# Kernel optimization log

Hardware: AMD Instinct MI355X
Metric: run time of the kernel (lower is better)

Reference implementation:

```python
import jax, jax.numpy as jnp
import numpy as np

C_IN = 128
C_INNER = 128


def setup_inputs() -> dict:
    key = jax.random.key(0)
    ks = jax.random.split(key, 9)
    b, c, h, w = 4, C_IN, 64, 64
    s = 1.0 / np.sqrt(c)
    x = jax.random.normal(ks[0], (b, c, h, w), dtype=jnp.float32)
    Wq = jax.random.normal(ks[1], (C_INNER, C_IN), dtype=jnp.float32) * s
    bq = jnp.zeros((C_INNER,), dtype=jnp.float32)
    Wk = jax.random.normal(ks[2], (C_INNER, C_IN), dtype=jnp.float32) * s
    bk = jnp.zeros((C_INNER,), dtype=jnp.float32)
    Wv = jax.random.normal(ks[3], (C_INNER, C_IN), dtype=jnp.float32) * s
    bv = jnp.zeros((C_INNER,), dtype=jnp.float32)
    Wo = jax.random.normal(ks[4], (C_IN, C_INNER), dtype=jnp.float32) * (1.0 / np.sqrt(C_INNER))
    bo = jnp.zeros((C_IN,), dtype=jnp.float32)
    return {"x": x, "Wq": Wq, "bq": bq, "Wk": Wk, "bk": bk,
            "Wv": Wv, "bv": bv, "Wo": Wo, "bo": bo}


def _conv1x1(x, W, bias):
    # x: (b,c,h,w), W: (o,c) -> (b,o,h,w)
    return jnp.einsum('oc,bchw->bohw', W, x) + bias[None, :, None, None]


def reference(x, Wq, bq, Wk, bk, Wv, bv, Wo, bo):
    b, c, h, w = x.shape
    ci = Wq.shape[0]
    n = h * w
    q = _conv1x1(x, Wq, bq).reshape(b, ci, n)          # (b, ci, n)
    k = _conv1x1(x, Wk, bk).reshape(b, ci, n)          # (b, ci, n)
    v = _conv1x1(x, Wv, bv).reshape(b, ci, n)          # (b, ci, n)
    # attn = softmax(q^T @ k) over keys
    attn = jnp.einsum('bci,bcj->bij', q, k)            # (b, n, n)
    attn = jax.nn.softmax(attn, axis=-1)
    out = jnp.einsum('bij,bcj->bci', attn, v)          # (b, ci, n)
    out = out.reshape(b, ci, h, w)
    out = _conv1x1(out, Wo, bo)
    return out + x
```

## Files before the change

### kernel.cpp

```cpp
#include <hip/hip_runtime.h>
#include <math.h>
#include <stdint.h>

#define CDIM 128
#define NTOT 4096
#define LOG2E 1.44269504f

typedef _Float16 f16x8 __attribute__((ext_vector_type(8)));
typedef float floatx4 __attribute__((ext_vector_type(4)));

static __device__ __forceinline__ floatx4 mfma16(f16x8 a, f16x8 b, floatx4 c) {
    return __builtin_amdgcn_mfma_f32_16x16x32_f16(a, b, c, 0, 0, 0);
}
static __device__ __forceinline__ unsigned short f2h(float f) {
    _Float16 h = (_Float16)f;
    return __builtin_bit_cast(unsigned short, h);
}
static __device__ __forceinline__ float h2f(unsigned short u) {
    return (float)__builtin_bit_cast(_Float16, u);
}
static __device__ __forceinline__ float fexp2(float x) {
#if __has_builtin(__builtin_amdgcn_exp2f)
    return __builtin_amdgcn_exp2f(x);
#else
    return exp2f(x);
#endif
}

#define SWZ(row, cc) ((((row) << 7)) + ((((cc) ^ ((row) & 15))) << 3))
#define SWZ8(row, cc) ((((row) << 6)) + ((((cc) ^ ((row) & 7))) << 3))

static __device__ __forceinline__ void gload_lds16(const void* g, void* l) {
    __builtin_amdgcn_global_load_lds(
        (const __attribute__((address_space(1))) void*)g,
        (__attribute__((address_space(3))) void*)l, 16, 0, 0);
}

__global__ __launch_bounds__(256) void qkv_proj_kernel(
    const float* __restrict__ x,
    const float* __restrict__ Wq, const float* __restrict__ Wk,
    const float* __restrict__ Wv,
    const float* __restrict__ bq, const float* __restrict__ bk,
    const float* __restrict__ bv,
    unsigned short* __restrict__ qo, unsigned short* __restrict__ ko,
    unsigned short* __restrict__ vo)
{
    __shared__ __align__(16) unsigned short Xs[64][136];
    __shared__ __align__(16) unsigned short Ws[3][64][136];

    const int t = threadIdx.x, b = blockIdx.y, n0 = blockIdx.x * 64;
    const int zo = blockIdx.z * 64;
    const int w = t >> 6, quad = (t >> 4) & 3, l15 = t & 15;

    {
        const int n = (t & 15) * 4;
        const int c = (t >> 4) * 8;
        float4 xr[8];
        #pragma unroll
        for (int j = 0; j < 8; ++j)
            xr[j] = *(const float4*)&x[((size_t)b * CDIM + c + j) * NTOT + n0 + n];
        #pragma unroll
        for (int k = 0; k < 4; ++k) {
            ushort4 ulo, uhi;
            ulo.x = f2h(((const float*)&xr[0])[k]);
            ulo.y = f2h(((const float*)&xr[1])[k]);
            ulo.z = f2h(((const float*)&xr[2])[k]);
            ulo.w = f2h(((const float*)&xr[3])[k]);
            uhi.x = f2h(((const float*)&xr[4])[k]);
            uhi.y = f2h(((const float*)&xr[5])[k]);
            uhi.z = f2h(((const float*)&xr[6])[k]);
            uhi.w = f2h(((const float*)&xr[7])[k]);
            *(ushort4*)&Xs[n + k][c]     = ulo;
            *(ushort4*)&Xs[n + k][c + 4] = uhi;
        }
    }
    {
        const int o = t >> 2, ch = (t & 3) * 32;
        #pragma unroll
        for (int s = 0; s < 3; ++s) {
            const float* W = (s == 0) ? Wq : (s == 1) ? Wk : Wv;
            #pragma unroll
            for (int i = 0; i < 8; ++i) {
                float4 f4 = *(const float4*)&W[(size_t)(zo + o) * CDIM + ch + i * 4];
                ushort4 u = { f2h(f4.x), f2h(f4.y), f2h(f4.z), f2h(f4.w) };
                *(ushort4*)&Ws[s][o][ch + i * 4] = u;
            }
        }
    }
    __syncthreads();

    f16x8 xf[4];
    #pragma unroll
    for (int f = 0; f < 4; ++f)
        xf[f] = *(const f16x8*)&Xs[w * 16 + l15][f * 32 + quad * 8];

    #pragma unroll
    for (int s = 0; s < 2; ++s) {
        const float* bias = s ? bk : bq;
        unsigned short* dst = s ? ko : qo;
        const float sc = (s == 0) ? LOG2E : 1.0f;
        #pragma unroll
        for (int ot = 0; ot < 4; ++ot) {
            floatx4 acc = (floatx4){0.f, 0.f, 0.f, 0.f};
            #pragma unroll
            for (int f = 0; f < 4; ++f) {
                f16x8 aW = *(const f16x8*)&Ws[s][ot * 16 + l15][f * 32 + quad * 8];
                acc = mfma16(aW, xf[f], acc);
            }
            const int ob = zo + ot * 16 + quad * 4;
            ushort4 u;
            u.x = f2h((acc[0] + bias[ob + 0]) * sc);
            u.y = f2h((acc[1] + bias[ob + 1]) * sc);
            u.z = f2h((acc[2] + bias[ob + 2]) * sc);
            u.w = f2h((acc[3] + bias[ob + 3]) * sc);
            *(ushort4*)&dst[((size_t)b * NTOT + n0 + w * 16 + l15) * CDIM + ob] = u;
        }
    }
    #pragma unroll
    for (int ot = 0; ot < 4; ++ot) {
        floatx4 acc = (floatx4){0.f, 0.f, 0.f, 0.f};
        #pragma unroll
        for (int f = 0; f < 4; ++f) {
            f16x8 bW = *(const f16x8*)&Ws[2][ot * 16 + l15][f * 32 + quad * 8];
            acc = mfma16(xf[f], bW, acc);
        }
        const int o = zo + ot * 16 + l15;
        const float bv_ = bv[o];
        ushort4 u;
        u.x = f2h(acc[0] + bv_); u.y = f2h(acc[1] + bv_);
        u.z = f2h(acc[2] + bv_); u.w = f2h(acc[3] + bv_);
        *(ushort4*)&vo[((size_t)b * CDIM + o) * NTOT + n0 + w * 16 + quad * 4] = u;
    }
}

__global__ __launch_bounds__(256, 2) void attn_kernel(
    const unsigned short* __restrict__ qg,
    const unsigned short* __restrict__ kg,
    const unsigned short* __restrict__ vg,
    unsigned short* __restrict__ Op,
    float* __restrict__ Ms, float* __restrict__ Ls)
{
    __shared__ __align__(16) unsigned short Kb[2][64 * 128];
    __shared__ __align__(16) unsigned short Vb[2][128 * 64];
    __shared__ __align__(16) unsigned short Ps[128 * 64];

    const int t = threadIdx.x;
    const int w = t >> 6, quad = (t >> 4) & 3, l15 = t & 15;

    const int bid = blockIdx.x;
    const int swz = ((bid & 7) << 6) | (bid >> 3);
    const int gidx = swz >> 5;
    const int b = gidx & 3;
    const int z = gidx >> 2;
    const int i0 = (swz & 31) * 128;
    const int jbase = z * 1024;
    const size_t vbase = (size_t)b * CDIM * NTOT;

    f16x8 bQ[2][4];
    #pragma unroll
    for (int nt = 0; nt < 2; ++nt) {
        const size_t qrow = ((size_t)b * NTOT + i0 + w * 32 + nt * 16 + l15) * CDIM;
        #pragma unroll
        for (int f = 0; f < 4; ++f)
            bQ[nt][f] = *(const f16x8*)&qg[qrow + f * 32 + quad * 8];
    }

    auto stageK = [&](unsigned short* Kd, int j0) {
        const size_t kbase = ((size_t)b * NTOT + j0) * CDIM;
        #pragma unroll
        for (int r = 0; r < 4; ++r) {
            const int flat = r * 256 + t;
            const int ldsoff = (r * 256 + (t & ~63)) * 8;
            const int krow = flat >> 4, kcc = flat & 15;
            gload_lds16(&kg[kbase + (size_t)krow * CDIM + ((kcc ^ (krow & 15)) << 3)],
                        &Kd[ldsoff]);
        }
    };
    auto stageV = [&](unsigned short* Vd, int j0) {
        const size_t vrow0 = vbase + j0;
        #pragma unroll
        for (int r = 0; r < 4; ++r) {
            const int flat = r * 256 + t;
            const int ldsoff = (r * 256 + (t & ~63)) * 8;
            const int vrow = flat >> 3, vcc = flat & 7;
            gload_lds16(&vg[vrow0 + (size_t)vrow * NTOT + ((vcc ^ (vrow & 7)) << 3)],
                        &Vd[ldsoff]);
        }
    };

    floatx4 accO[2][8];
    #pragma unroll
    for (int nt = 0; nt < 2; ++nt)
        #pragma unroll
        for (int dt = 0; dt < 8; ++dt) accO[nt][dt] = (floatx4){0.f, 0.f, 0.f, 0.f};
    float m_run[2] = {-INFINITY, -INFINITY};
    float l_part[2] = {0.f, 0.f};

    floatx4 accT[2][4];
    uint2 pu[2][4];
    f16x8 bP[2][2];

    auto QK = [&](const unsigned short* Kd) {
        #pragma unroll
        for (int nt = 0; nt < 2; ++nt)
            #pragma unroll
            for (int jt = 0; jt < 4; ++jt) accT[nt][jt] = (floatx4){0.f, 0.f, 0.f, 0.f};
        __builtin_amdgcn_s_setprio(1);
        #pragma unroll
        for (int jt = 0; jt < 4; ++jt)
            #pragma unroll
            for (int f = 0; f < 4; ++f) {
                f16x8 aK = *(const f16x8*)&Kd[SWZ(jt * 16 + l15, f * 4 + quad)];
                accT[0][jt] = mfma16(aK, bQ[0][f], accT[0][jt]);
                accT[1][jt] = mfma16(aK, bQ[1][f], accT[1][jt]);
            }
        __builtin_amdgcn_s_setprio(0);
    };
    auto RB = [&]() {
        #pragma unroll
        for (int nt = 0; nt < 2; ++nt) {
            const int prow = w * 32 + nt * 16 + l15;
            #pragma unroll
            for (int kb = 0; kb < 2; ++kb)
                bP[nt][kb] = *(const f16x8*)&Ps[SWZ8(prow, kb * 4 + quad)];
        }
    };
    auto PV = [&](const unsigned short* Vd) {
        __builtin_amdgcn_s_setprio(1);
        #pragma unroll
        for (int dt = 0; dt < 8; ++dt)
            #pragma unroll
            for (int kb = 0; kb < 2; ++kb) {
                f16x8 aV = *(const f16x8*)&Vd[SWZ8(dt * 16 + l15, kb * 4 + quad)];
                accO[0][dt] = mfma16(aV, bP[0][kb], accO[0][dt]);
                accO[1][dt] = mfma16(aV, bP[1][kb], accO[1][dt]);
            }
        __builtin_amdgcn_s_setprio(0);
    };
    auto SM = [&]() {
        #pragma unroll
        for (int nt = 0; nt < 2; ++nt) {
            float tm = accT[nt][0][0];
            #pragma unroll
            for (int jt = 0; jt < 4; ++jt)
                #pragma unroll
                for (int r = 0; r < 4; ++r) tm = fmaxf(tm, accT[nt][jt][r]);
            tm = fmaxf(tm, __shfl_xor(tm, 16));
            tm = fmaxf(tm, __shfl_xor(tm, 32));
            if (__ballot(tm > m_run[nt] + 11.5416f)) {
                const float m_new = fmaxf(m_run[nt], tm);
                const float alpha = fexp2(m_run[nt] - m_new);
                m_run[nt] = m_new;
                l_part[nt] *= alpha;
                #pragma unroll
                for (int dt = 0; dt < 8; ++dt) {
                    accO[nt][dt][0] *= alpha; accO[nt][dt][1] *= alpha;
                    accO[nt][dt][2] *= alpha; accO[nt][dt][3] *= alpha;
                }
            }
            const float mcur = m_run[nt];
            float ps = 0.f;
            #pragma unroll
            for (int jt = 0; jt < 4; ++jt) {
                float p0 = fexp2(accT[nt][jt][0] - mcur);
                float p1 = fexp2(accT[nt][jt][1] - mcur);
                float p2 = fexp2(accT[nt][jt][2] - mcur);
                float p3 = fexp2(accT[nt][jt][3] - mcur);
                ps += (p0 + p1) + (p2 + p3);
                pu[nt][jt].x = __builtin_bit_cast(unsigned int,
                                   __builtin_amdgcn_cvt_pkrtz(p0, p1));
                pu[nt][jt].y = __builtin_bit_cast(unsigned int,
                                   __builtin_amdgcn_cvt_pkrtz(p2, p3));
            }
            l_part[nt] += ps;
        }
    };
    auto WP = [&]() {
        #pragma unroll
        for (int nt = 0; nt < 2; ++nt) {
            const int prow = w * 32 + nt * 16 + l15;
            #pragma unroll
            for (int jt = 0; jt < 4; ++jt)
                *(uint2*)&Ps[SWZ8(prow, 2 * jt + (quad >> 1)) + (quad & 1) * 4] =
                    pu[nt][jt];
        }
    };

    stageK(Kb[0], jbase);
    stageV(Vb[0], jbase);
    unsigned short *Kc = Kb[0], *Kn = Kb[1], *Vc = Vb[0], *Vn = Vb[1];

    asm volatile("s_waitcnt vmcnt(0) lgkmcnt(0)" ::: "memory");
    __builtin_amdgcn_s_barrier();
    stageK(Kn, jbase + 64);
    stageV(Vn, jbase + 64);
    QK(Kc);
    SM();
    WP();
    { unsigned short* tp = Kc; Kc = Kn; Kn = tp; tp = Vc; Vc = Vn; Vn = tp; }

    for (int it = 1; it <= 14; ++it) {
        asm volatile("s_waitcnt vmcnt(4) lgkmcnt(0)" ::: "memory");
        __builtin_amdgcn_s_barrier();
        RB();
        stageK(Kn, jbase + (it + 1) * 64);
        QK(Kc);
        PV(Vn);
        SM();
        asm volatile("s_waitcnt lgkmcnt(0)" ::: "memory");
        __builtin_amdgcn_s_barrier();
        stageV(Vn, jbase + (it + 1) * 64);
        WP();
        { unsigned short* tp = Kc; Kc = Kn; Kn = tp; tp = Vc; Vc = Vn; Vn = tp; }
    }

    asm volatile("s_waitcnt vmcnt(4) lgkmcnt(0)" ::: "memory");
    __builtin_amdgcn_s_barrier();
    RB();
    QK(Kc);
    PV(Vn);
    SM();
    WP();
    asm volatile("s_waitcnt vmcnt(0)" ::: "memory");
    __builtin_amdgcn_s_barrier();
    RB();
    PV(Vc);

    #pragma unroll
    for (int nt = 0; nt < 2; ++nt) {
        float lf = l_part[nt];
        lf += __shfl_xor(lf, 16);
        lf += __shfl_xor(lf, 32);
        const float inv = 1.0f / lf;
        const size_t orow =
            (((size_t)z * 4 + b) * NTOT + i0 + w * 32 + nt * 16 + l15) * CDIM;
        #pragma unroll
        for (int dt = 0; dt < 8; ++dt) {
            ushort4 u;
            u.x = f2h(accO[nt][dt][0] * inv); u.y = f2h(accO[nt][dt][1] * inv);
            u.z = f2h(accO[nt][dt][2] * inv); u.w = f2h(accO[nt][dt][3] * inv);
            *(ushort4*)&Op[orow + dt * 16 + quad * 4] = u;
        }
        if (quad == 0) {
            const int idx = (z * 4 + b) * NTOT + i0 + w * 32 + nt * 16 + l15;
            Ms[idx] = m_run[nt];
            Ls[idx] = lf;
        }
    }
}

__global__ __launch_bounds__(256) void out_proj_kernel(
    const unsigned short* __restrict__ Op,
    const float* __restrict__ Ms, const float* __restrict__ Ls,
    const float* __restrict__ Wo, const float* __restrict__ bo,
    const float* __restrict__ x, float* __restrict__ out)
{
    __shared__ __align__(16) unsigned short As[64][136];
    __shared__ __align__(16) unsigned short Ws[64][136];

    const int t = threadIdx.x, b = blockIdx.y, n0 = blockIdx.x * 64;
    const int zo = blockIdx.z * 64;
    const int w = t >> 6, quad = (t >> 4) & 3, l15 = t & 15;

    const size_t PER = (size_t)NTOT * 4 * CDIM;

    #pragma unroll
    for (int r = 0; r < 4; ++r) {
        int flat = r * 256 + t;
        int row = flat >> 4, c16 = (flat & 15) * 8;
        const int bn = b * NTOT + n0 + row;
        float m0 = Ms[bn], m1 = Ms[bn + 16384], m2 = Ms[bn + 32768], m3 = Ms[bn + 49152];
        float M = fmaxf(fmaxf(m0, m1), fmaxf(m2, m3));
        float w0 = Ls[bn]         * fexp2(m0 - M);
        float w1 = Ls[bn + 16384] * fexp2(m1 - M);
        float w2 = Ls[bn + 32768] * fexp2(m2 - M);
        float w3 = Ls[bn + 49152] * fexp2(m3 - M);
        const float inv = 1.0f / (w0 + w1 + w2 + w3);
        w0 *= inv; w1 *= inv; w2 *= inv; w3 *= inv;

        const size_t base = (size_t)bn * CDIM + c16;
        uint4 a0 = *(const uint4*)&Op[base];
        uint4 a1 = *(const uint4*)&Op[PER + base];
        uint4 a2 = *(const uint4*)&Op[2 * PER + base];
        uint4 a3 = *(const uint4*)&Op[3 * PER + base];
        const unsigned short* p0 = (const unsigned short*)&a0;
        const unsigned short* p1 = (const unsigned short*)&a1;
        const unsigned short* p2 = (const unsigned short*)&a2;
        const unsigned short* p3 = (const unsigned short*)&a3;
        unsigned short mv[8];
        #pragma unroll
        for (int j = 0; j < 8; ++j)
            mv[j] = f2h(w0 * h2f(p0[j]) + w1 * h2f(p1[j]) +
                        w2 * h2f(p2[j]) + w3 * h2f(p3[j]));
        *(uint4*)&As[row][c16] = *(const uint4*)mv;
    }
    {
        int o = t >> 2, ch = (t & 3) * 32;
        #pragma unroll
        for (int i = 0; i < 8; ++i) {
            float4 f4 = *(const float4*)&Wo[(size_t)(zo + o) * CDIM + ch + i * 4];
            ushort4 u = { f2h(f4.x), f2h(f4.y), f2h(f4.z), f2h(f4.w) };
            *(ushort4*)&Ws[o][ch + i * 4] = u;
        }
    }
    __syncthreads();

    f16x8 bA[4];
    #pragma unroll
    for (int f = 0; f < 4; ++f)
        bA[f] = *(const f16x8*)&As[w * 16 + l15][f * 32 + quad * 8];

    #pragma unroll
    for (int ot = 0; ot < 4; ++ot) {
        floatx4 acc = (floatx4){0.f, 0.f, 0.f, 0.f};
        #pragma unroll
        for (int f = 0; f < 4; ++f) {
            f16x8 aW = *(const f16x8*)&Ws[ot * 16 + l15][f * 32 + quad * 8];
            acc = mfma16(aW, bA[f], acc);
        }
        const int ob = zo + ot * 16 + quad * 4;
        #pragma unroll
        for (int r = 0; r < 4; ++r) {
            size_t idx = ((size_t)b * CDIM + ob + r) * NTOT + n0 + w * 16 + l15;
            out[idx] = acc[r] + bo[ob + r] + x[idx];
        }
    }
}

extern "C" void kernel_launch(void* const* d_in, const int* in_sizes, int n_in,
                              void* d_out, int out_size, void* d_ws, size_t ws_size,
                              hipStream_t stream)
{
    const float* x  = (const float*)d_in[0];
    const float* Wq = (const float*)d_in[1];
    const float* bq = (const float*)d_in[2];
    const float* Wk = (const float*)d_in[3];
    const float* bk = (const float*)d_in[4];
    const float* Wv = (const float*)d_in[5];
    const float* bv = (const float*)d_in[6];
    const float* Wo = (const float*)d_in[7];
    const float* bo = (const float*)d_in[8];
    float* out = (float*)d_out;

    const size_t PER = (size_t)4 * CDIM * NTOT;
    unsigned short* q_ws  = (unsigned short*)d_ws;
    unsigned short* k_ws  = q_ws + PER;
    unsigned short* v_ws  = k_ws + PER;
    unsigned short* op_ws = v_ws + PER;
    float*          ms_ws = (float*)(op_ws + 4 * PER);
    float*          ls_ws = ms_ws + 4 * 16384;

    qkv_proj_kernel<<<dim3(64, 4, 2), dim3(256), 0, stream>>>(
        x, Wq, Wk, Wv, bq, bk, bv, q_ws, k_ws, v_ws);
    attn_kernel<<<dim3(512), dim3(256), 0, stream>>>(
        q_ws, k_ws, v_ws, op_ws, ms_ws, ls_ws);
    out_proj_kernel<<<dim3(64, 4, 2), dim3(256), 0, stream>>>(
        op_ws, ms_ws, ls_ws, Wo, bo, x, out);
}
```

Measured before the change: 140.8 us.

## Split keys into eight chunks with smaller tiles to raise attention occupancy

```diff
diff --git a/kernel.cpp b/kernel.cpp
--- a/kernel.cpp
+++ b/kernel.cpp
@@ -5,6 +5,8 @@
 #define CDIM 128
 #define NTOT 4096
 #define LOG2E 1.44269504f
+#define NZ 8
+#define KT 32
 
 typedef _Float16 f16x8 __attribute__((ext_vector_type(8)));
 typedef float floatx4 __attribute__((ext_vector_type(4)));
@@ -133,27 +135,27 @@
     }
 }
 
-__global__ __launch_bounds__(256, 2) void attn_kernel(
+__global__ __launch_bounds__(256, 4) void attn_kernel(
     const unsigned short* __restrict__ qg,
     const unsigned short* __restrict__ kg,
     const unsigned short* __restrict__ vg,
     unsigned short* __restrict__ Op,
     float* __restrict__ Ms, float* __restrict__ Ls)
 {
-    __shared__ __align__(16) unsigned short Kb[2][64 * 128];
-    __shared__ __align__(16) unsigned short Vb[2][128 * 64];
-    __shared__ __align__(16) unsigned short Ps[128 * 64];
+    __shared__ __align__(16) unsigned short Kb[2][KT * 128];
+    __shared__ __align__(16) unsigned short Vb[2][64 * 64];
+    __shared__ __align__(16) unsigned short Ps[64 * 64];
 
     const int t = threadIdx.x;
     const int w = t >> 6, quad = (t >> 4) & 3, l15 = t & 15;
 
     const int bid = blockIdx.x;
-    const int swz = ((bid & 7) << 6) | (bid >> 3);
+    const int swz = ((bid & 7) << 7) | (bid >> 3);
     const int gidx = swz >> 5;
     const int b = gidx & 3;
     const int z = gidx >> 2;
     const int i0 = (swz & 31) * 128;
-    const int jbase = z * 1024;
+    const int jbase = z * (NTOT / NZ);
     const size_t vbase = (size_t)b * CDIM * NTOT;
 
     f16x8 bQ[2][4];
@@ -168,7 +170,7 @@
     auto stageK = [&](unsigned short* Kd, int j0) {
         const size_t kbase = ((size_t)b * NTOT + j0) * CDIM;
         #pragma unroll
-        for (int r = 0; r < 4; ++r) {
+        for (int r = 0; r < 2; ++r) {
             const int flat = r * 256 + t;
             const int ldsoff = (r * 256 + (t & ~63)) * 8;
             const int krow = flat >> 4, kcc = flat & 15;
@@ -177,14 +179,14 @@
         }
     };
     auto stageV = [&](unsigned short* Vd, int j0) {
-        const size_t vrow0 = vbase + j0;
-        #pragma unroll
-        for (int r = 0; r < 4; ++r) {
+        #pragma unroll
+        for (int r = 0; r < 2; ++r) {
             const int flat = r * 256 + t;
             const int ldsoff = (r * 256 + (t & ~63)) * 8;
-            const int vrow = flat >> 3, vcc = flat & 7;
-            gload_lds16(&vg[vrow0 + (size_t)vrow * NTOT + ((vcc ^ (vrow & 7)) << 3)],
-                        &Vd[ldsoff]);
+            const int vrow = flat >> 3, s = flat & 7;
+            const int cc = s ^ (vrow & 7);
+            const int d = vrow * 2 + (cc >> 2), jc = cc & 3;
+            gload_lds16(&vg[vbase + (size_t)d * NTOT + j0 + jc * 8], &Vd[ldsoff]);
         }
     };
 
@@ -196,18 +198,18 @@
     float m_run[2] = {-INFINITY, -INFINITY};
     float l_part[2] = {0.f, 0.f};
 
-    floatx4 accT[2][4];
-    uint2 pu[2][4];
-    f16x8 bP[2][2];
+    floatx4 accT[2][2];
+    uint2 pu[2][2];
+    f16x8 bP[2];
 
     auto QK = [&](const unsigned short* Kd) {
         #pragma unroll
         for (int nt = 0; nt < 2; ++nt)
             #pragma unroll
-            for (int jt = 0; jt < 4; ++jt) accT[nt][jt] = (floatx4){0.f, 0.f, 0.f, 0.f};
+            for (int jt = 0; jt < 2; ++jt) accT[nt][jt] = (floatx4){0.f, 0.f, 0.f, 0.f};
         __builtin_amdgcn_s_setprio(1);
         #pragma unroll
-        for (int jt = 0; jt < 4; ++jt)
+        for (int jt = 0; jt < 2; ++jt)
             #pragma unroll
             for (int f = 0; f < 4; ++f) {
                 f16x8 aK = *(const f16x8*)&Kd[SWZ(jt * 16 + l15, f * 4 + quad)];
@@ -219,22 +221,19 @@
     auto RB = [&]() {
         #pragma unroll
         for (int nt = 0; nt < 2; ++nt) {
-            const int prow = w * 32 + nt * 16 + l15;
-            #pragma unroll
-            for (int kb = 0; kb < 2; ++kb)
-                bP[nt][kb] = *(const f16x8*)&Ps[SWZ8(prow, kb * 4 + quad)];
+            const int q = w * 32 + nt * 16 + l15;
+            bP[nt] = *(const f16x8*)&Ps[SWZ8(q >> 1, ((q & 1) << 2) + quad)];
         }
     };
     auto PV = [&](const unsigned short* Vd) {
         __builtin_amdgcn_s_setprio(1);
         #pragma unroll
-        for (int dt = 0; dt < 8; ++dt)
-            #pragma unroll
-            for (int kb = 0; kb < 2; ++kb) {
-                f16x8 aV = *(const f16x8*)&Vd[SWZ8(dt * 16 + l15, kb * 4 + quad)];
-                accO[0][dt] = mfma16(aV, bP[0][kb], accO[0][dt]);
-                accO[1][dt] = mfma16(aV, bP[1][kb], accO[1][dt]);
-            }
+        for (int dt = 0; dt < 8; ++dt) {
+            const int d = dt * 16 + l15;
+            f16x8 aV = *(const f16x8*)&Vd[SWZ8(d >> 1, ((d & 1) << 2) + quad)];
+            accO[0][dt] = mfma16(aV, bP[0], accO[0][dt]);
+            accO[1][dt] = mfma16(aV, bP[1], accO[1][dt]);
+        }
         __builtin_amdgcn_s_setprio(0);
     };
     auto SM = [&]() {
@@ -242,7 +241,7 @@
         for (int nt = 0; nt < 2; ++nt) {
             float tm = accT[nt][0][0];
             #pragma unroll
-            for (int jt = 0; jt < 4; ++jt)
+            for (int jt = 0; jt < 2; ++jt)
                 #pragma unroll
                 for (int r = 0; r < 4; ++r) tm = fmaxf(tm, accT[nt][jt][r]);
             tm = fmaxf(tm, __shfl_xor(tm, 16));
@@ -261,7 +260,7 @@
             const float mcur = m_run[nt];
             float ps = 0.f;
             #pragma unroll
-            for (int jt = 0; jt < 4; ++jt) {
+            for (int jt = 0; jt < 2; ++jt) {
                 float p0 = fexp2(accT[nt][jt][0] - mcur);
                 float p1 = fexp2(accT[nt][jt][1] - mcur);
                 float p2 = fexp2(accT[nt][jt][2] - mcur);
@@ -278,11 +277,11 @@
     auto WP = [&]() {
         #pragma unroll
         for (int nt = 0; nt < 2; ++nt) {
-            const int prow = w * 32 + nt * 16 + l15;
-            #pragma unroll
-            for (int jt = 0; jt < 4; ++jt)
-                *(uint2*)&Ps[SWZ8(prow, 2 * jt + (quad >> 1)) + (quad & 1) * 4] =
-                    pu[nt][jt];
+            const int q = w * 32 + nt * 16 + l15;
+            #pragma unroll
+            for (int jt = 0; jt < 2; ++jt)
+                *(uint2*)&Ps[SWZ8(q >> 1, ((q & 1) << 2) + jt * 2 + (quad >> 1))
+                             + (quad & 1) * 4] = pu[nt][jt];
         }
     };
 
@@ -292,29 +291,29 @@
 
     asm volatile("s_waitcnt vmcnt(0) lgkmcnt(0)" ::: "memory");
     __builtin_amdgcn_s_barrier();
-    stageK(Kn, jbase + 64);
-    stageV(Vn, jbase + 64);
+    stageK(Kn, jbase + KT);
+    stageV(Vn, jbase + KT);
     QK(Kc);
     SM();
     WP();
     { unsigned short* tp = Kc; Kc = Kn; Kn = tp; tp = Vc; Vc = Vn; Vn = tp; }
 
     for (int it = 1; it <= 14; ++it) {
-        asm volatile("s_waitcnt vmcnt(4) lgkmcnt(0)" ::: "memory");
+        asm volatile("s_waitcnt vmcnt(2) lgkmcnt(0)" ::: "memory");
         __builtin_amdgcn_s_barrier();
         RB();
-        stageK(Kn, jbase + (it + 1) * 64);
+        stageK(Kn, jbase + (it + 1) * KT);
         QK(Kc);
         PV(Vn);
         SM();
         asm volatile("s_waitcnt lgkmcnt(0)" ::: "memory");
         __builtin_amdgcn_s_barrier();
-        stageV(Vn, jbase + (it + 1) * 64);
+        stageV(Vn, jbase + (it + 1) * KT);
         WP();
         { unsigned short* tp = Kc; Kc = Kn; Kn = tp; tp = Vc; Vc = Vn; Vn = tp; }
     }
 
-    asm volatile("s_waitcnt vmcnt(4) lgkmcnt(0)" ::: "memory");
+    asm volatile("s_waitcnt vmcnt(2) lgkmcnt(0)" ::: "memory");
     __builtin_amdgcn_s_barrier();
     RB();
     QK(Kc);
@@ -369,29 +368,31 @@
         int flat = r * 256 + t;
         int row = flat >> 4, c16 = (flat & 15) * 8;
         const int bn = b * NTOT + n0 + row;
-        float m0 = Ms[bn], m1 = Ms[bn + 16384], m2 = Ms[bn + 32768], m3 = Ms[bn + 49152];
-        float M = fmaxf(fmaxf(m0, m1), fmaxf(m2, m3));
-        float w0 = Ls[bn]         * fexp2(m0 - M);
-        float w1 = Ls[bn + 16384] * fexp2(m1 - M);
-        float w2 = Ls[bn + 32768] * fexp2(m2 - M);
-        float w3 = Ls[bn + 49152] * fexp2(m3 - M);
-        const float inv = 1.0f / (w0 + w1 + w2 + w3);
-        w0 *= inv; w1 *= inv; w2 *= inv; w3 *= inv;
+
+        float m[NZ], lw[NZ];
+        float M = -INFINITY;
+        #pragma unroll
+        for (int zz = 0; zz < NZ; ++zz) { m[zz] = Ms[bn + zz * 16384]; M = fmaxf(M, m[zz]); }
+        float wsum = 0.f;
+        #pragma unroll
+        for (int zz = 0; zz < NZ; ++zz) {
+            lw[zz] = Ls[bn + zz * 16384] * fexp2(m[zz] - M);
+            wsum += lw[zz];
+        }
+        const float inv = 1.0f / wsum;
 
         const size_t base = (size_t)bn * CDIM + c16;
-        uint4 a0 = *(const uint4*)&Op[base];
-        uint4 a1 = *(const uint4*)&Op[PER + base];
-        uint4 a2 = *(const uint4*)&Op[2 * PER + base];
-        uint4 a3 = *(const uint4*)&Op[3 * PER + base];
-        const unsigned short* p0 = (const unsigned short*)&a0;
-        const unsigned short* p1 = (const unsigned short*)&a1;
-        const unsigned short* p2 = (const unsigned short*)&a2;
-        const unsigned short* p3 = (const unsigned short*)&a3;
+        float acc[8] = {0.f, 0.f, 0.f, 0.f, 0.f, 0.f, 0.f, 0.f};
+        #pragma unroll
+        for (int zz = 0; zz < NZ; ++zz) {
+            uint4 a = *(const uint4*)&Op[zz * PER + base];
+            const unsigned short* p = (const unsigned short*)&a;
+            #pragma unroll
+            for (int j = 0; j < 8; ++j) acc[j] += lw[zz] * h2f(p[j]);
+        }
         unsigned short mv[8];
         #pragma unroll
-        for (int j = 0; j < 8; ++j)
-            mv[j] = f2h(w0 * h2f(p0[j]) + w1 * h2f(p1[j]) +
-                        w2 * h2f(p2[j]) + w3 * h2f(p3[j]));
+        for (int j = 0; j < 8; ++j) mv[j] = f2h(acc[j] * inv);
         *(uint4*)&As[row][c16] = *(const uint4*)mv;
     }
     {
@@ -447,12 +448,12 @@
     unsigned short* k_ws  = q_ws + PER;
     unsigned short* v_ws  = k_ws + PER;
     unsigned short* op_ws = v_ws + PER;
-    float*          ms_ws = (float*)(op_ws + 4 * PER);
-    float*          ls_ws = ms_ws + 4 * 16384;
+    float*          ms_ws = (float*)(op_ws + (size_t)NZ * PER);
+    float*          ls_ws = ms_ws + (size_t)NZ * 16384;
 
     qkv_proj_kernel<<<dim3(64, 4, 2), dim3(256), 0, stream>>>(
         x, Wq, Wk, Wv, bq, bk, bv, q_ws, k_ws, v_ws);
-    attn_kernel<<<dim3(512), dim3(256), 0, stream>>>(
+    attn_kernel<<<dim3(1024), dim3(256), 0, stream>>>(
         q_ws, k_ws, v_ws, op_ws, ms_ws, ls_ws);
     out_proj_kernel<<<dim3(64, 4, 2), dim3(256), 0, stream>>>(
         op_ws, ms_ws, ls_ws, Wo, bo, x, out);
```

Measured after the change: 249.2 us. +77.0%, slower.
